# Performance work log

Hardware: AMD Instinct MI355X
Metric: run time of the kernel (lower is better)

The kernel has to match this reference:

```python
import jax, jax.numpy as jnp
import numpy as np

B, S, H = 4, 1024, 2560          # batch, seq, hidden_size
E, K, F = 32, 6, 1536            # num_experts, top_k, moe_intermediate_size
SHARED_F = 2 * 1536              # moe_num_shared_experts * moe_intermediate_size
NORM_MIN = 1e-12                 # config.moe_norm_min


def setup_inputs() -> dict:
    key = jax.random.key(0)
    ks = jax.random.split(key, 9)
    rnd = lambda k, shape, scale=0.02: jax.random.normal(k, shape, dtype=jnp.float32) * scale
    return {
        "hidden_states": jax.random.normal(ks[0], (B, S, H), dtype=jnp.float32),
        "router_w": rnd(ks[1], (E, H)),              # Ernie4_5_MoeTopKRouter.weight (fp32)
        "router_bias": jnp.zeros((E,), jnp.float32),  # moe_statics.e_score_correction_bias
        "gate_w": rnd(ks[2], (E, H, F)),
        "up_w": rnd(ks[3], (E, H, F)),
        "down_w": rnd(ks[4], (E, F, H)),
        "shared_gate_w": rnd(ks[5], (H, SHARED_F)),
        "shared_up_w": rnd(ks[6], (H, SHARED_F)),
        "shared_down_w": rnd(ks[7], (SHARED_F, H)),
    }


def _mlp(x, gw, uw, dw):
    # Ernie4_5_MoeMLP: down( silu(gate(x)) * up(x) ), no biases
    return (jax.nn.silu(x @ gw) * (x @ uw)) @ dw


def _forward(hidden_states, router_w, router_bias, gate_w, up_w, down_w,
             shared_gate_w, shared_up_w, shared_down_w):
    T = B * S
    xt = hidden_states.reshape(T, H)

    # shared experts path (always-on dense MLP)
    shared_out = _mlp(xt, shared_gate_w, shared_up_w, shared_down_w)

    # router: fp32 linear -> softmax -> (+ correction bias) -> top-k -> renorm
    logits = xt.astype(jnp.float32) @ router_w.T            # [T, E]
    probs = jax.nn.softmax(logits, axis=-1)
    top_w, top_i = jax.lax.top_k(probs + router_bias[None, :], K)  # [T, K]
    top_w = top_w / jnp.clip(jnp.sum(top_w, axis=-1, keepdims=True), NORM_MIN)
    top_w = top_w.astype(hidden_states.dtype)

    # expert combine: loop over the fixed expert set; per-token combine weight
    # cw[t] = sum_k top_w[t,k] * (top_i[t,k] == e)  (matches one-hot dispatch +
    # index_add_ scatter combine of the original)
    out = jnp.zeros_like(xt)
    for e in range(E):
        cw = jnp.sum(jnp.where(top_i == e, top_w, 0.0), axis=-1)  # [T]
        y = _mlp(xt, gate_w[e], up_w[e], down_w[e])               # [T, H]
        out = out + cw[:, None] * y

    out = out + shared_out
    return out.reshape(B, S, H)


def reference(hidden_states, router_w, router_bias, gate_w, up_w, down_w,
              shared_gate_w, shared_up_w, shared_down_w):
    return _forward(hidden_states, router_w, router_bias, gate_w, up_w, down_w,
                    shared_gate_w, shared_up_w, shared_down_w)
```

## Files before the change

### kernel.cpp

```cpp
#include <hip/hip_runtime.h>
#include <hip/hip_bf16.h>
#include <math.h>

#define T_TOK 4096
#define HID   2560
#define NEXP  32
#define KTOP  6
#define FF    1536
#define SFF   3072
#define MAXP  (T_TOK*KTOP)

typedef __attribute__((ext_vector_type(8))) short short8;
typedef __attribute__((ext_vector_type(4))) float f32x4;

static __device__ __forceinline__ unsigned short f2bf(float x){
  return __builtin_bit_cast(unsigned short, (__bf16)x);
}
static __device__ __forceinline__ float bf2f(unsigned short u){
  unsigned int x = ((unsigned int)u) << 16;
  return __builtin_bit_cast(float, x);
}

static __device__ __forceinline__ void gload_lds16(const void* g, void* l){
  __builtin_amdgcn_global_load_lds(
      (const __attribute__((address_space(1))) unsigned int*)g,
      (__attribute__((address_space(3))) unsigned int*)l, 16, 0, 0);
}

__global__ void k_cast_x(const float* __restrict__ x, unsigned short* __restrict__ xb){
  int i = (blockIdx.x * 256 + threadIdx.x) * 4;
  float4 v = *(const float4*)(x + i);
  ushort4 o;
  o.x = f2bf(v.x); o.y = f2bf(v.y); o.z = f2bf(v.z); o.w = f2bf(v.w);
  *(ushort4*)(xb + i) = o;
}

__global__ __launch_bounds__(256)
void k_transpose(const float* __restrict__ in, unsigned short* __restrict__ out,
                 const int R, const int C, const long long outBS){
  const size_t bi = (size_t)blockIdx.z * (size_t)R * C;
  const size_t bo = (size_t)blockIdx.z * (size_t)outBS;
  __shared__ unsigned short t2[64][72];
  const int r0 = blockIdx.y * 64, c0 = blockIdx.x * 64;
  const int tid = threadIdx.x;
  const int cr = tid & 15;
  const int rr = tid >> 4;
#pragma unroll
  for (int i = 0; i < 4; ++i){
    const int r = rr + 16*i;
    float4 v = *(const float4*)(in + bi + (size_t)(r0 + r)*C + c0 + cr*4);
    ushort4 p;
    p.x = f2bf(v.x); p.y = f2bf(v.y); p.z = f2bf(v.z); p.w = f2bf(v.w);
    *(ushort4*)(&t2[r][cr*4]) = p;
  }
  __syncthreads();
  const int rw = tid & 7;
  const int ro = tid >> 3;
#pragma unroll
  for (int i = 0; i < 2; ++i){
    const int c = ro + 32*i;
    ushort4 a, b;
    a.x = t2[rw*8+0][c]; a.y = t2[rw*8+1][c]; a.z = t2[rw*8+2][c]; a.w = t2[rw*8+3][c];
    b.x = t2[rw*8+4][c]; b.y = t2[rw*8+5][c]; b.z = t2[rw*8+6][c]; b.w = t2[rw*8+7][c];
    unsigned short* op = out + bo + (size_t)(c0 + c)*R + r0 + rw*8;
    *(ushort4*)(op)     = a;
    *(ushort4*)(op + 4) = b;
  }
}

__global__ void k_router(const float* __restrict__ x, const float* __restrict__ rw,
                         const float* __restrict__ rb, float* __restrict__ top_w,
                         int* __restrict__ top_i, int* __restrict__ counts){
  const int lane = threadIdx.x & 63;
  const int wv   = threadIdx.x >> 6;
  const int t    = blockIdx.x * 4 + wv;
  const float* xr = x + (size_t)t * HID;
  float xv[40];
#pragma unroll
  for (int i = 0; i < 40; ++i) xv[i] = xr[lane + 64*i];
  float sc[32];
  for (int e = 0; e < 32; ++e){
    const float* w = rw + (size_t)e * HID;
    float s = 0.f;
#pragma unroll
    for (int i = 0; i < 40; ++i) s = fmaf(xv[i], w[lane + 64*i], s);
#pragma unroll
    for (int o = 32; o; o >>= 1) s += __shfl_xor(s, o);
    sc[e] = s;
  }
  float mx = sc[0];
#pragma unroll
  for (int e = 1; e < 32; ++e) mx = fmaxf(mx, sc[e]);
  float se = 0.f;
#pragma unroll
  for (int e = 0; e < 32; ++e){ sc[e] = expf(sc[e] - mx); se += sc[e]; }
  const float inv = 1.f / se;
#pragma unroll
  for (int e = 0; e < 32; ++e) sc[e] = sc[e] * inv + rb[e];

  unsigned chosen = 0; float swv[KTOP]; int sid[KTOP]; float wsum = 0.f;
#pragma unroll
  for (int k = 0; k < KTOP; ++k){
    float bv = -1e30f; int bi = 0;
#pragma unroll
    for (int e = 0; e < 32; ++e){
      bool ok = !((chosen >> e) & 1u);
      if (ok && sc[e] > bv){ bv = sc[e]; bi = e; }
    }
    chosen |= 1u << bi; swv[k] = bv; sid[k] = bi; wsum += bv;
  }
  const float dn = fmaxf(wsum, 1e-12f);
  if (lane < KTOP){
    top_w[t*KTOP + lane] = swv[lane] / dn;
    top_i[t*KTOP + lane] = sid[lane];
    atomicAdd(counts + sid[lane], 1);
  }
}

__global__ void k_scan(const int* __restrict__ counts, int* __restrict__ offsets){
  if (threadIdx.x == 0){
    int a = 0;
    for (int e = 0; e < NEXP; ++e){ offsets[e] = a; a += counts[e]; }
    offsets[NEXP] = a;
  }
}

__global__ void k_scatter(const int* __restrict__ top_i, const float* __restrict__ top_w,
                          const int* __restrict__ offsets, int* __restrict__ cursor,
                          int* __restrict__ pair_tok, float* __restrict__ pair_w){
  const int t = blockIdx.x * 256 + threadIdx.x;
  if (t >= T_TOK) return;
#pragma unroll
  for (int k = 0; k < KTOP; ++k){
    int e = top_i[t*KTOP + k];
    int pos = offsets[e] + atomicAdd(cursor + e, 1);
    pair_tok[pos] = t;
    pair_w[pos]   = top_w[t*KTOP + k];
  }
}

template<int F8>
__global__ __launch_bounds__(256)
void k_swiglu(const unsigned short* __restrict__ y, unsigned short* __restrict__ act){
  const int i = blockIdx.x * 256 + threadIdx.x;
  const int p = i / F8, c = i % F8;
  const unsigned short* row = y + (size_t)p * (2*F8*8);
  short8 g8 = *(const short8*)(row + c*8);
  short8 u8 = *(const short8*)(row + F8*8 + c*8);
  short8 o;
#pragma unroll
  for (int j = 0; j < 8; ++j){
    float g = bf2f((unsigned short)g8[j]);
    float u = bf2f((unsigned short)u8[j]);
    float s = (g / (1.f + expf(-g))) * u;
    o[j] = (short)f2bf(s);
  }
  *(short8*)(act + (size_t)p*F8*8 + c*8) = o;
}

template<bool GROUPED, bool GATHER, int OUT>
__global__ __launch_bounds__(512, 2)
void k_gemm(const unsigned short* __restrict__ A,
            const unsigned short* __restrict__ BT,
            void* __restrict__ outp,
            const int* __restrict__ pair_tok, const float* __restrict__ pair_w,
            const int* __restrict__ counts, const int* __restrict__ offsets,
            const int N, const int K, const int ntiles)
{
  const int NT = K >> 6;
  const int total = gridDim.x;
  const int phys  = blockIdx.x;
  const int logical = (phys & 7) * (total >> 3) + (phys >> 3);
  const int mt   = logical & 15;
  const int rest = logical >> 4;
  const int n0 = (rest % ntiles) << 8;
  const int e  = rest / ntiles;

  int M, base;
  if (GROUPED){ M = counts[e]; base = offsets[e]; }
  else        { M = T_TOK;     base = 0; }
  if (mt * 256 >= M) return;
  const unsigned short* Bb = BT + (size_t)e * (size_t)N * K;

  __shared__ unsigned short AS[4*8192];
  __shared__ unsigned short BS[4*8192];

  const int tid  = threadIdx.x;
  const int lane = tid & 63;
  const int w    = tid >> 6;
  const int wr = w >> 2, wc = w & 3;

  const int lrow = lane >> 2, lchunk = lane & 3;
  const int swz = (lchunk ^ ((lrow >> 1) & 3)) * 8;
  const unsigned short *ap0, *ap1, *bp0, *bp1;
  {
    const int r0 = w*32 + lrow, r1 = w*32 + 16 + lrow;
    int i0 = min(mt*256 + r0, M - 1);
    int i1 = min(mt*256 + r1, M - 1);
    int rowA0 = GATHER ? pair_tok[base + i0] : (GROUPED ? base + i0 : i0);
    int rowA1 = GATHER ? pair_tok[base + i1] : (GROUPED ? base + i1 : i1);
    ap0 = A + (size_t)rowA0 * K + swz;
    ap1 = A + (size_t)rowA1 * K + swz;
    bp0 = Bb + (size_t)(n0 + r0) * K + swz;
    bp1 = Bb + (size_t)(n0 + r1) * K + swz;
  }

  const f32x4 zero = {0.f,0.f,0.f,0.f};
  f32x4 acc[8][4];
#pragma unroll
  for (int m = 0; m < 8; ++m)
#pragma unroll
    for (int n = 0; n < 4; ++n) acc[m][n] = zero;

  const int fr = lane & 15;
  const int fg = ((lane >> 4) ^ ((lane >> 1) & 3)) * 16;
  short8 af[8], bf[4];

#define STAGE(h)                                                            \
  { const int _s = (h) & 3; const int _k = (h) * 32;                        \
    gload_lds16(ap0 + _k, (char*)AS + _s*16384 + (w*32)*64);                \
    gload_lds16(ap1 + _k, (char*)AS + _s*16384 + (w*32+16)*64);             \
    gload_lds16(bp0 + _k, (char*)BS + _s*16384 + (w*32)*64);                \
    gload_lds16(bp1 + _k, (char*)BS + _s*16384 + (w*32+16)*64); }

#define FRAGS(SLOT)                                                         \
  { const char* _as = (const char*)AS + (SLOT)*16384;                       \
    const char* _bs = (const char*)BS + (SLOT)*16384;                       \
    _Pragma("unroll")                                                       \
    for (int m = 0; m < 8; ++m)                                             \
      af[m] = *(const short8*)(_as + (wr*128 + m*16 + fr)*64 + fg);         \
    _Pragma("unroll")                                                       \
    for (int n = 0; n < 4; ++n)                                             \
      bf[n] = *(const short8*)(_bs + (wc*64 + n*16 + fr)*64 + fg); }

#define MFMAS                                                               \
  __builtin_amdgcn_s_setprio(1);                                            \
  _Pragma("unroll")                                                         \
  for (int m = 0; m < 8; ++m)                                               \
  _Pragma("unroll")                                                         \
  for (int n = 0; n < 4; ++n)                                               \
    acc[m][n] = __builtin_amdgcn_mfma_f32_16x16x32_bf16(af[m], bf[n], acc[m][n], 0, 0, 0); \
  __builtin_amdgcn_s_setprio(0);

  STAGE(0) STAGE(1) STAGE(2)
  asm volatile("s_waitcnt vmcnt(8)" ::: "memory");
  __builtin_amdgcn_s_barrier();
  __builtin_amdgcn_sched_barrier(0);

  for (int t = 0; t < NT; ++t){
    const int sA = (2*t) & 3, sB = (2*t + 1) & 3;
    FRAGS(sA)
    if (2*t + 3 < 2*NT) STAGE(2*t + 3)
    __builtin_amdgcn_s_barrier();
    __builtin_amdgcn_sched_barrier(0);
    MFMAS
    if (t + 1 < NT) asm volatile("s_waitcnt vmcnt(8)" ::: "memory");
    else            asm volatile("s_waitcnt vmcnt(0)" ::: "memory");
    __builtin_amdgcn_s_barrier();
    __builtin_amdgcn_sched_barrier(0);
    FRAGS(sB)
    if (2*t + 4 < 2*NT) STAGE(2*t + 4)
    __builtin_amdgcn_s_barrier();
    __builtin_amdgcn_sched_barrier(0);
    MFMAS
    if (t + 2 < NT){
      asm volatile("s_waitcnt vmcnt(8)" ::: "memory");
      __builtin_amdgcn_s_barrier();
      __builtin_amdgcn_sched_barrier(0);
    } else if (t + 1 < NT){
      asm volatile("s_waitcnt vmcnt(4)" ::: "memory");
      __builtin_amdgcn_s_barrier();
      __builtin_amdgcn_sched_barrier(0);
    }
  }
#undef STAGE
#undef FRAGS
#undef MFMAS

#pragma unroll
  for (int m = 0; m < 8; ++m)
#pragma unroll
    for (int j = 0; j < 4; ++j){
      const int rr = mt*256 + wr*128 + m*16 + (lane >> 4)*4 + j;
      if (rr < M){
        const int col = n0 + wc*64 + (lane & 15);
        if (OUT == 0){
          unsigned short* orow = (unsigned short*)outp + (size_t)(base + rr) * N + col;
#pragma unroll
          for (int n = 0; n < 4; ++n) orow[n*16] = f2bf(acc[m][n][j]);
        } else if (OUT == 1){
          const int p = base + rr;
          const int tok = pair_tok[p];
          const float pw = pair_w[p];
          float* orow = (float*)outp + (size_t)tok * HID + col;
#pragma unroll
          for (int n = 0; n < 4; ++n) atomicAdd(orow + n*16, acc[m][n][j] * pw);
        } else {
          float* orow = (float*)outp + (size_t)rr * N + col;
#pragma unroll
          for (int n = 0; n < 4; ++n) orow[n*16] = acc[m][n][j];
        }
      }
    }
}

extern "C" void kernel_launch(void* const* d_in, const int* in_sizes, int n_in,
                              void* d_out, int out_size, void* d_ws, size_t ws_size,
                              hipStream_t stream)
{
  (void)in_sizes; (void)n_in; (void)out_size; (void)ws_size;
  const float* hid = (const float*)d_in[0];
  const float* rw  = (const float*)d_in[1];
  const float* rb  = (const float*)d_in[2];
  const float* gw  = (const float*)d_in[3];
  const float* uw  = (const float*)d_in[4];
  const float* dw  = (const float*)d_in[5];
  const float* sgw = (const float*)d_in[6];
  const float* suw = (const float*)d_in[7];
  const float* sdw = (const float*)d_in[8];
  float* out = (float*)d_out;

  char* ws = (char*)d_ws;
  size_t o = 0;
  unsigned short* xb   = (unsigned short*)(ws + o); o += (size_t)T_TOK*HID*2;
  unsigned short* act  = (unsigned short*)(ws + o); o += (size_t)MAXP*FF*2;
  unsigned short* sact = (unsigned short*)(ws + o); o += (size_t)T_TOK*SFF*2;
  unsigned short* y    = (unsigned short*)(ws + o); o += (size_t)MAXP*2*FF*2;
  unsigned short* sy   = (unsigned short*)(ws + o); o += (size_t)T_TOK*2*SFF*2;
  unsigned short* Wbuf = (unsigned short*)(ws + o);
  unsigned short* guT  = Wbuf;
  unsigned short* sguT = Wbuf + (size_t)NEXP*2*FF*HID;
  unsigned short* dT   = Wbuf;
  unsigned short* sdT  = Wbuf + (size_t)NEXP*HID*FF;
  o += (size_t)NEXP*2*FF*HID*2 + (size_t)2*SFF*HID*2;
  float* top_w    = (float*)(ws + o); o += (size_t)T_TOK*KTOP*4;
  int*   top_i    = (int*)(ws + o);   o += (size_t)T_TOK*KTOP*4;
  float* pair_w   = (float*)(ws + o); o += (size_t)MAXP*4;
  int*   pair_tok = (int*)(ws + o);   o += (size_t)MAXP*4;
  int*   counts   = (int*)(ws + o);   o += NEXP*4;
  int*   offsets  = (int*)(ws + o);   o += (NEXP+1)*4;
  int*   cursor   = (int*)(ws + o);   o += NEXP*4;

  hipMemsetAsync(counts, 0, (NEXP + (NEXP+1) + NEXP) * sizeof(int), stream);

  k_cast_x<<<(T_TOK*HID)/1024, 256, 0, stream>>>(hid, xb);
  k_router<<<T_TOK/4, 256, 0, stream>>>(hid, rw, rb, top_w, top_i, counts);
  k_scan<<<1, 64, 0, stream>>>(counts, offsets);
  k_scatter<<<T_TOK/256, 256, 0, stream>>>(top_i, top_w, offsets, cursor, pair_tok, pair_w);

  k_transpose<<<dim3(FF/64,  HID/64, NEXP), 256, 0, stream>>>(gw,  guT,                    HID, FF,  (long long)2*FF*HID);
  k_transpose<<<dim3(FF/64,  HID/64, NEXP), 256, 0, stream>>>(uw,  guT + (size_t)FF*HID,   HID, FF,  (long long)2*FF*HID);
  k_transpose<<<dim3(SFF/64, HID/64, 1),    256, 0, stream>>>(sgw, sguT,                   HID, SFF, 0);
  k_transpose<<<dim3(SFF/64, HID/64, 1),    256, 0, stream>>>(suw, sguT + (size_t)SFF*HID, HID, SFF, 0);

  k_gemm<true,  true,  0><<<16*(2*FF/256)*NEXP, 512, 0, stream>>>(
      xb, guT, y, pair_tok, nullptr, counts, offsets, 2*FF, HID, 2*FF/256);
  k_gemm<false, false, 0><<<16*(2*SFF/256), 512, 0, stream>>>(
      xb, sguT, sy, nullptr, nullptr, nullptr, nullptr, 2*SFF, HID, 2*SFF/256);
  k_swiglu<FF/8><<<(MAXP*(FF/8))/256, 256, 0, stream>>>(y, act);
  k_swiglu<SFF/8><<<(T_TOK*(SFF/8))/256, 256, 0, stream>>>(sy, sact);

  k_transpose<<<dim3(HID/64, FF/64,  NEXP), 256, 0, stream>>>(dw,  dT,  FF,  HID, (long long)HID*FF);
  k_transpose<<<dim3(HID/64, SFF/64, 1),    256, 0, stream>>>(sdw, sdT, SFF, HID, 0);

  k_gemm<false, false, 2><<<16*(HID/256), 512, 0, stream>>>(
      sact, sdT, out, nullptr, nullptr, nullptr, nullptr, HID, SFF, HID/256);
  k_gemm<true,  false, 1><<<16*(HID/256)*NEXP, 512, 0, stream>>>(
      act, dT, out, pair_tok, pair_w, counts, offsets, HID, FF, HID/256);
}
```

Before: 1.902 ms.

## Split GEMM main loop into half-M phases with separate A/B staging

Restructures the GEMM k-loop so that each 32-wide k slice is processed in two half-M phases. Each phase loads 4 A fragments plus 4 shared B fragments from LDS, then runs 16 MFMAs, with A and B global-to-LDS loads issued in separate phases. The aim is to cut live fragment registers and interleave memory issue with MFMA work more finely. In exchange there are more barriers per k slice, and the vmcnt accounting changes, which risks stalls or races if the counts are off.

New measurement: 1.942 ms. 2.1% more time.

```diff
diff --git a/kernel.cpp b/kernel.cpp
--- a/kernel.cpp
+++ b/kernel.cpp
@@ -167,7 +167,7 @@
             const int* __restrict__ counts, const int* __restrict__ offsets,
             const int N, const int K, const int ntiles)
 {
-  const int NT = K >> 6;
+  const int NH = K >> 5;
   const int total = gridDim.x;
   const int phys  = blockIdx.x;
   const int logical = (phys & 7) * (total >> 3) + (phys >> 3);
@@ -214,68 +214,65 @@
 
   const int fr = lane & 15;
   const int fg = ((lane >> 4) ^ ((lane >> 1) & 3)) * 16;
-  short8 af[8], bf[4];
-
-#define STAGE(h)                                                            \
-  { const int _s = (h) & 3; const int _k = (h) * 32;                        \
+
+#define STAGE_A(h)                                                          \
+  { const int _s = (h) & 3; const size_t _k = (size_t)(h) * 32;             \
     gload_lds16(ap0 + _k, (char*)AS + _s*16384 + (w*32)*64);                \
-    gload_lds16(ap1 + _k, (char*)AS + _s*16384 + (w*32+16)*64);             \
+    gload_lds16(ap1 + _k, (char*)AS + _s*16384 + (w*32+16)*64); }
+#define STAGE_B(h)                                                          \
+  { const int _s = (h) & 3; const size_t _k = (size_t)(h) * 32;             \
     gload_lds16(bp0 + _k, (char*)BS + _s*16384 + (w*32)*64);                \
     gload_lds16(bp1 + _k, (char*)BS + _s*16384 + (w*32+16)*64); }
 
-#define FRAGS(SLOT)                                                         \
-  { const char* _as = (const char*)AS + (SLOT)*16384;                       \
-    const char* _bs = (const char*)BS + (SLOT)*16384;                       \
-    _Pragma("unroll")                                                       \
-    for (int m = 0; m < 8; ++m)                                             \
-      af[m] = *(const short8*)(_as + (wr*128 + m*16 + fr)*64 + fg);         \
-    _Pragma("unroll")                                                       \
-    for (int n = 0; n < 4; ++n)                                             \
-      bf[n] = *(const short8*)(_bs + (wc*64 + n*16 + fr)*64 + fg); }
-
-#define MFMAS                                                               \
-  __builtin_amdgcn_s_setprio(1);                                            \
-  _Pragma("unroll")                                                         \
-  for (int m = 0; m < 8; ++m)                                               \
-  _Pragma("unroll")                                                         \
-  for (int n = 0; n < 4; ++n)                                               \
-    acc[m][n] = __builtin_amdgcn_mfma_f32_16x16x32_bf16(af[m], bf[n], acc[m][n], 0, 0, 0); \
-  __builtin_amdgcn_s_setprio(0);
-
-  STAGE(0) STAGE(1) STAGE(2)
+  STAGE_A(0) STAGE_B(0) STAGE_A(1) STAGE_B(1) STAGE_A(2) STAGE_B(2)
   asm volatile("s_waitcnt vmcnt(8)" ::: "memory");
   __builtin_amdgcn_s_barrier();
   __builtin_amdgcn_sched_barrier(0);
 
-  for (int t = 0; t < NT; ++t){
-    const int sA = (2*t) & 3, sB = (2*t + 1) & 3;
-    FRAGS(sA)
-    if (2*t + 3 < 2*NT) STAGE(2*t + 3)
+  for (int h = 0; h < NH; ++h){
+    const int s = h & 3;
+    const char* _as = (const char*)AS + s*16384;
+    const char* _bs = (const char*)BS + s*16384;
+    short8 bq[4], af[4];
+#pragma unroll
+    for (int n = 0; n < 4; ++n)
+      bq[n] = *(const short8*)(_bs + (wc*64 + n*16 + fr)*64 + fg);
+#pragma unroll
+    for (int m = 0; m < 4; ++m)
+      af[m] = *(const short8*)(_as + (wr*128 + m*16 + fr)*64 + fg);
+    if (h + 3 < NH) STAGE_A(h + 3)
     __builtin_amdgcn_s_barrier();
     __builtin_amdgcn_sched_barrier(0);
-    MFMAS
-    if (t + 1 < NT) asm volatile("s_waitcnt vmcnt(8)" ::: "memory");
-    else            asm volatile("s_waitcnt vmcnt(0)" ::: "memory");
+    __builtin_amdgcn_s_setprio(1);
+#pragma unroll
+    for (int m = 0; m < 4; ++m)
+#pragma unroll
+      for (int n = 0; n < 4; ++n)
+        acc[m][n] = __builtin_amdgcn_mfma_f32_16x16x32_bf16(af[m], bq[n], acc[m][n], 0, 0, 0);
+    __builtin_amdgcn_s_setprio(0);
     __builtin_amdgcn_s_barrier();
     __builtin_amdgcn_sched_barrier(0);
-    FRAGS(sB)
-    if (2*t + 4 < 2*NT) STAGE(2*t + 4)
+#pragma unroll
+    for (int m = 0; m < 4; ++m)
+      af[m] = *(const short8*)(_as + (wr*128 + (m+4)*16 + fr)*64 + fg);
+    if (h + 3 < NH) STAGE_B(h + 3)
     __builtin_amdgcn_s_barrier();
     __builtin_amdgcn_sched_barrier(0);
-    MFMAS
-    if (t + 2 < NT){
-      asm volatile("s_waitcnt vmcnt(8)" ::: "memory");
-      __builtin_amdgcn_s_barrier();
-      __builtin_amdgcn_sched_barrier(0);
-    } else if (t + 1 < NT){
-      asm volatile("s_waitcnt vmcnt(4)" ::: "memory");
-      __builtin_amdgcn_s_barrier();
-      __builtin_amdgcn_sched_barrier(0);
-    }
-  }
-#undef STAGE
-#undef FRAGS
-#undef MFMAS
+    __builtin_amdgcn_s_setprio(1);
+#pragma unroll
+    for (int m = 0; m < 4; ++m)
+#pragma unroll
+      for (int n = 0; n < 4; ++n)
+        acc[m+4][n] = __builtin_amdgcn_mfma_f32_16x16x32_bf16(af[m], bq[n], acc[m+4][n], 0, 0, 0);
+    __builtin_amdgcn_s_setprio(0);
+    if (h + 3 < NH)      asm volatile("s_waitcnt vmcnt(8)" ::: "memory");
+    else if (h + 2 < NH) asm volatile("s_waitcnt vmcnt(4)" ::: "memory");
+    else if (h + 1 < NH) asm volatile("s_waitcnt vmcnt(0)" ::: "memory");
+    __builtin_amdgcn_s_barrier();
+    __builtin_amdgcn_sched_barrier(0);
+  }
+#undef STAGE_A
+#undef STAGE_B
 
 #pragma unroll
   for (int m = 0; m < 8; ++m)
```
